# Kernel optimization log

Hardware: AMD Instinct MI355X
Metric: run time of the kernel (lower is better)

The kernel has to match this reference:

```python
import jax, jax.numpy as jnp
import numpy as np

# ---- module geometry ----
BULK = 64          # bulk (J2) integration points, 3 comps each
COH = 32           # cohesive integration points, 2 comps each
LS = BULK * 3 + COH * 2  # = 256, material layer width

# ---- J2 plasticity material constants (plane-stress, linear isotropic hardening) ----
E_MOD = 200.0
NU = 0.3
SY0 = 2.0
HARD = 10.0
G_MOD = E_MOD / (2.0 * (1.0 + NU))
_c = E_MOD / (1.0 - NU * NU)
C_EL = np.array([[_c, _c * NU, 0.0], [_c * NU, _c, 0.0], [0.0, 0.0, _c * (1.0 - NU) / 2.0]], dtype=np.float32)
C_INV = np.linalg.inv(C_EL).astype(np.float32)

# ---- Turon cohesive-zone constants (bilinear damage law) ----
K_PEN = 50.0       # penalty stiffness
DELTA0 = 0.1       # damage-onset effective jump
DELTAF = 1.0       # full-failure effective jump


def j2_update(eps, epsp, epbar):
    # eps, epsp: [B,P,3]; epbar: [B,P]. Radial-return with linear hardening.
    sig_tr = jnp.einsum('bpi,ji->bpj', eps - epsp, jnp.asarray(C_EL))
    s1, s2, s12 = sig_tr[..., 0], sig_tr[..., 1], sig_tr[..., 2]
    seq = jnp.sqrt(jnp.maximum(s1 * s1 - s1 * s2 + s2 * s2 + 3.0 * s12 * s12, 1e-12))
    f = seq - (SY0 + HARD * epbar)
    plastic = f > 0.0
    dep = jnp.where(plastic, f / (3.0 * G_MOD + HARD), 0.0)
    r = (SY0 + HARD * (epbar + dep)) / seq
    sig = jnp.where(plastic[..., None], r[..., None] * sig_tr, sig_tr)
    epsp_new = jnp.where(plastic[..., None], eps - jnp.einsum('bpj,ij->bpi', sig, jnp.asarray(C_INV)), epsp)
    return sig, epsp_new, epbar + dep


def coh_update(jump, hist):
    # jump: [B,P,2] (normal, shear); hist: [B,P] max effective jump (damage history).
    dn, ds = jump[..., 0], jump[..., 1]
    lam = jnp.sqrt(jnp.maximum(jnp.maximum(dn, 0.0) ** 2 + ds * ds, 1e-12))
    hist_new = jnp.maximum(hist, lam)
    dmg = jnp.clip(DELTAF * (hist_new - DELTA0) / (jnp.maximum(hist_new, 1e-12) * (DELTAF - DELTA0)), 0.0, 1.0)
    tn = K_PEN * dn * jnp.where(dn > 0.0, 1.0 - dmg, 1.0)  # compression is undamaged
    ts = (1.0 - dmg) * K_PEN * ds
    return jnp.stack([tn, ts], axis=-1), hist_new


def setup_inputs() -> dict:
    key = jax.random.key(0)
    k1, k2, k3 = jax.random.split(key, 3)
    x = jax.random.normal(k1, (256, 1024, 16), dtype=jnp.float32)
    W1 = jax.random.normal(k2, (LS, 16), dtype=jnp.float32) * 0.1
    W2 = jax.random.normal(k3, (16, LS), dtype=jnp.float32) * 0.1
    return {"x": x, "W1": W1, "W2": W2}


def reference(x, W1, W2):
    B, T, F = x.shape
    # fc1 applied to every (batch, time) slice (original loops; here one GEMM)
    h = jnp.einsum('btf,lf->btl', x, W1)  # [B,T,LS]
    h_t = jnp.transpose(h, (1, 0, 2))     # [T,B,LS] for the time scan

    epsp0 = jnp.zeros((B, BULK, 3), dtype=x.dtype)
    epbar0 = jnp.zeros((B, BULK), dtype=x.dtype)
    hist0 = jnp.zeros((B, COH), dtype=x.dtype)

    def step(carry, ht):
        epsp, epbar, hist = carry
        eps = ht[:, : BULK * 3].reshape(B, BULK, 3)
        jmp = ht[:, BULK * 3:].reshape(B, COH, 2)
        sig, epsp, epbar = j2_update(eps, epsp, epbar)   # update + commit per step
        trac, hist = coh_update(jmp, hist)
        y = jnp.concatenate([sig.reshape(B, -1), trac.reshape(B, -1)], axis=-1)
        return (epsp, epbar, hist), y

    _, ys = jax.lax.scan(step, (epsp0, epbar0, hist0), h_t)  # [T,B,LS]
    ys = jnp.transpose(ys, (1, 0, 2))  # [B,T,LS]
    # softLayer fc2: linear with softplus-constrained (non-negative) weights
    out = jnp.einsum('btl,ol->bto', ys, jax.nn.softplus(W2))
    return out
```

## Files before the change

### kernel.cpp

```cpp
#include <hip/hip_runtime.h>
#include <cmath>
#include <cstdint>

#define BATCH  256
#define TT     1024
#define FIN    16
#define TC     32
#define NCHUNK (TT / TC)
#define SROW   328
#define YSS    336

typedef __attribute__((ext_vector_type(8))) short short8;
typedef __attribute__((ext_vector_type(4))) float floatx4;

__device__ __forceinline__ unsigned short f2bf_rne(float f) {
    union { float f; unsigned int i; } v; v.f = f;
    unsigned int b = v.i;
    return (unsigned short)((b + 0x7FFFu + ((b >> 16) & 1u)) >> 16);
}
__device__ __forceinline__ float u2f(unsigned int u) {
    union { unsigned int i; float f; } v; v.i = u; return v.f;
}

#define BARRIER() asm volatile("s_waitcnt lgkmcnt(0)\n\ts_barrier" ::: "memory")

#define MC00   219.78021978021977f
#define MC01   65.93406593406593f
#define MC22   76.92307692307692f
#define MSY0   2.0f
#define AK     0.958466453674121406f
#define BK     0.041533546325878594f


__global__ __launch_bounds__(512, 1)
void fused_mat_kernel(const float* __restrict__ x,
                      const float* __restrict__ w1,
                      const float* __restrict__ w2,
                      float* __restrict__ out)
{
    __shared__ __attribute__((aligned(16))) float          s_h[2][TC][SROW];
    __shared__ __attribute__((aligned(16))) unsigned short s_y[2][TC][YSS];

    const int tid  = threadIdx.x;
    const int b    = blockIdx.x;
    const int lane = tid & 63;
    const int wv   = tid >> 6;
    const int m    = lane & 15;
    const int q    = lane >> 4;

    const size_t xrow = (size_t)b * TT;

    const bool isG     = (wv == 3) | (wv == 4) | (wv == 7);
    const int  hw      = (wv == 3) ? 0 : (wv == 4) ? 1 : 2;
    const int  nbase   = hw * 8;
    const int  nfrag   = (hw == 2) ? 4 : 8;
    const bool useDelta = (hw < 2);

    short8 wfrag[8];
    short8 vf[10];
    uint4  rxc[2][2], rxp[2][2];

    auto emit = [&](const short8* af, float* dst) {
        #pragma unroll
        for (int mt = 0; mt < 2; ++mt) {
            float* drow = dst + (mt * 16 + m) * SROW + q * 4 + nbase * 16;
            #pragma unroll
            for (int j = 0; j < 8; ++j) {
                if (j < nfrag) {
                    floatx4 acc = {0.f, 0.f, 0.f, 0.f};
                    acc = __builtin_amdgcn_mfma_f32_16x16x32_bf16(wfrag[j], af[mt], acc, 0, 0, 0);
                    *(floatx4*)(drow + j * 16) = acc;
                }
            }
        }
    };

    if (isG) {
        #pragma unroll
        for (int j = 0; j < 8; ++j) {
            short8 fr;
            #pragma unroll
            for (int jj = 0; jj < 8; ++jj) fr[jj] = 0;
            if (j < nfrag) {
                const int n = nbase + j;
                #pragma unroll
                for (int jj = 0; jj < 8; ++jj) {
                    float v = 0.f;
                    if (q < 2) {
                        const int f = q * 8 + jj;
                        if (n < 16) {
                            const int lp = n * 16 + m, c = lp >> 2, cm = lp & 3;
                            if (cm < 3) {
                                const float wa  = w1[(3 * c + 0) * FIN + f];
                                const float wb  = w1[(3 * c + 1) * FIN + f];
                                const float wcc = w1[(3 * c + 2) * FIN + f];
                                v = (cm == 0) ? fmaf(MC01, wb, MC00 * wa)
                                  : (cm == 1) ? fmaf(MC00, wb, MC01 * wa)
                                              : MC22 * wcc;
                            }
                        } else {
                            v = w1[(192 + (n - 16) * 16 + m) * FIN + f];
                        }
                    }
                    fr[jj] = (short)f2bf_rne(v);
                }
            }
            wfrag[j] = fr;
        }
        short8 af0[2];
        #pragma unroll
        for (int mt = 0; mt < 2; ++mt) {
            #pragma unroll
            for (int j = 0; j < 8; ++j) {
                float val = 0.f;
                if (q < 2) {
                    const int rowB = mt * 16 + m;
                    const float xc = x[(xrow + rowB) * FIN + q * 8 + j];
                    float xp = 0.f;
                    if (rowB > 0) xp = x[(xrow + rowB - 1) * FIN + q * 8 + j];
                    val = useDelta ? (xc - xp) : xc;
                }
                af0[mt][j] = (short)f2bf_rne(val);
            }
        }
        if (q < 2) {
            #pragma unroll
            for (int mt = 0; mt < 2; ++mt) {
                const int rowB = TC + mt * 16 + m;
                const float* xc = x + (xrow + rowB) * FIN + q * 8;
                const float* xp = x + (xrow + rowB - 1) * FIN + q * 8;
                rxc[mt][0] = *(const uint4*)xc;  rxc[mt][1] = *(const uint4*)(xc + 4);
                rxp[mt][0] = *(const uint4*)xp;  rxp[mt][1] = *(const uint4*)(xp + 4);
            }
        }
        emit(af0, &s_h[0][0][0]);
    } else if (wv == 5 || wv == 6) {
        #pragma unroll
        for (int ks = 0; ks < 10; ++ks) {
            #pragma unroll
            for (int j = 0; j < 8; ++j) {
                const int p = ks * 32 + q * 8 + j;
                unsigned short v = 0;
                if (p < 256) {
                    const int comp = p & 3;
                    if (comp < 3) {
                        const int l = 3 * (p >> 2) + comp;
                        float xv = w2[m * 256 + l];
                        float sp = fmaxf(xv, 0.0f) + log1pf(expf(-fabsf(xv)));
                        v = f2bf_rne(sp);
                    }
                } else {
                    const int l = p - 64;
                    float xv = w2[m * 256 + l];
                    float sp = fmaxf(xv, 0.0f) + log1pf(expf(-fabsf(xv)));
                    v = f2bf_rne(sp);
                }
                vf[ks][j] = (short)v;
            }
        }
    }

    float sg0 = 0.f, sg1 = 0.f, sg2 = 0.f, syv = MSY0, pre = AK * MSY0;
    float hist = 0.f;

    __syncthreads();

    for (int i = 0; i <= NCHUNK; ++i) {
        if (wv < 2) {
            if (i < NCHUNK && lane < 32) {
                const int p = wv * 32 + lane;
                const float* hb = &s_h[i & 1][0][0] + 4 * p;
                unsigned short* yb = &s_y[i & 1][0][0] + 4 * p;
                floatx4 dvv[TC];
                #pragma unroll
                for (int t = 0; t < TC; ++t) dvv[t] = *(const floatx4*)(hb + t * SROW);
                #pragma unroll
                for (int t = 0; t < TC; ++t) {
                    const floatx4 dv = dvv[t];
                    const float t0 = sg0 + dv.x, t1 = sg1 + dv.y, t2 = sg2 + dv.z;
                    const float s01 = t0 - t1;
                    const float u   = t2 * t2;
                    const float w3  = fmaf(u, 2.0f, u);
                    const float bb  = fmaf(t1, t1, w3);
                    const float qq  = fmaxf(fmaf(t0, s01, bb), 1e-12f);
                    const float rs  = __builtin_amdgcn_rsqf(qq);
                    const float seq = qq * rs;
                    const float rr  = fminf(fmaf(pre, rs, BK), 1.0f);
                    sg0 = rr * t0; sg1 = rr * t1; sg2 = rr * t2;
                    syv = fmaxf(syv, fmaf(BK, seq, pre));
                    pre = AK * syv;
                    unsigned int r0, r1;
                    asm("v_cvt_pk_bf16_f32 %0, %1, %2" : "=v"(r0) : "v"(sg0), "v"(sg1));
                    asm("v_cvt_pk_bf16_f32 %0, %1, %2" : "=v"(r1) : "v"(sg2), "v"(sg2));
                    uint2 pk; pk.x = r0; pk.y = r1;
                    *(uint2*)(yb + t * YSS) = pk;
                }
            }
        } else if (wv == 2) {
            if (i < NCHUNK && lane < 32) {
                const float* hc = &s_h[i & 1][0][0] + 256 + 2 * lane;
                unsigned short* yc = &s_y[i & 1][0][0] + 256 + 2 * lane;
                float2 jvv[TC];
                #pragma unroll
                for (int t = 0; t < TC; ++t) jvv[t] = *(const float2*)(hc + t * SROW);
                #pragma unroll
                for (int t = 0; t < TC; ++t) {
                    const float dn = jvv[t].x, ds = jvv[t].y;
                    const float dnp = fmaxf(dn, 0.0f);
                    const float lam = __builtin_amdgcn_sqrtf(fmaxf(fmaf(dnp, dnp, ds * ds), 1e-12f));
                    hist = fmaxf(hist, lam);
                    float dmg = (hist - 0.1f) * __builtin_amdgcn_rcpf(hist * 0.9f);
                    dmg = fminf(fmaxf(dmg, 0.0f), 1.0f);
                    const float om = 1.0f - dmg;
                    const float tn = 50.0f * dn * (dn > 0.0f ? om : 1.0f);
                    const float ts = om * 50.0f * ds;
                    unsigned int r;
                    asm("v_cvt_pk_bf16_f32 %0, %1, %2" : "=v"(r) : "v"(tn), "v"(ts));
                    *(unsigned int*)(yc + t * YSS) = r;
                }
            }
        } else if (isG) {
            if (i + 1 < NCHUNK) {
                short8 af[2];
                #pragma unroll
                for (int mt = 0; mt < 2; ++mt) {
                    const unsigned int wc[8] = {rxc[mt][0].x, rxc[mt][0].y, rxc[mt][0].z, rxc[mt][0].w,
                                                rxc[mt][1].x, rxc[mt][1].y, rxc[mt][1].z, rxc[mt][1].w};
                    const unsigned int wp[8] = {rxp[mt][0].x, rxp[mt][0].y, rxp[mt][0].z, rxp[mt][0].w,
                                                rxp[mt][1].x, rxp[mt][1].y, rxp[mt][1].z, rxp[mt][1].w};
                    #pragma unroll
                    for (int j = 0; j < 8; ++j) {
                        unsigned short v = 0;
                        if (q < 2) {
                            const float xc = u2f(wc[j]), xp = u2f(wp[j]);
                            const float val = useDelta ? (xc - xp) : xc;
                            v = f2bf_rne(val);
                        }
                        af[mt][j] = (short)v;
                    }
                }
                if (i + 2 < NCHUNK && q < 2) {
                    #pragma unroll
                    for (int mt = 0; mt < 2; ++mt) {
                        const int rowB = (i + 2) * TC + mt * 16 + m;
                        const float* xc = x + (xrow + rowB) * FIN + q * 8;
                        const float* xp = x + (xrow + rowB - 1) * FIN + q * 8;
                        rxc[mt][0] = *(const uint4*)xc;  rxc[mt][1] = *(const uint4*)(xc + 4);
                        rxp[mt][0] = *(const uint4*)xp;  rxp[mt][1] = *(const uint4*)(xp + 4);
                    }
                }
                emit(af, &s_h[(i + 1) & 1][0][0]);
            }
        } else {
            if (i >= 1) {
                const int mt = wv - 5;
                const int tb = (i - 1) * TC;
                const unsigned short* yb = &s_y[(i - 1) & 1][0][0];
                floatx4 a0 = {0.f, 0.f, 0.f, 0.f};
                floatx4 a1 = {0.f, 0.f, 0.f, 0.f};
                #pragma unroll
                for (int ks = 0; ks < 5; ++ks) {
                    const short8* yp = (const short8*)(yb + (mt * 16 + m) * YSS + ks * 32 + q * 8);
                    a0 = __builtin_amdgcn_mfma_f32_16x16x32_bf16(*yp, vf[ks], a0, 0, 0, 0);
                }
                #pragma unroll
                for (int ks = 5; ks < 10; ++ks) {
                    const short8* yp = (const short8*)(yb + (mt * 16 + m) * YSS + ks * 32 + q * 8);
                    a1 = __builtin_amdgcn_mfma_f32_16x16x32_bf16(*yp, vf[ks], a1, 0, 0, 0);
                }
                #pragma unroll
                for (int r = 0; r < 4; ++r)
                    out[(xrow + tb + mt * 16 + q * 4 + r) * FIN + m] = a0[r] + a1[r];
            }
        }
        BARRIER();
    }
}

extern "C" void kernel_launch(void* const* d_in, const int* in_sizes, int n_in,
                              void* d_out, int out_size, void* d_ws, size_t ws_size,
                              hipStream_t stream) {
    const float* x  = (const float*)d_in[0];
    const float* w1 = (const float*)d_in[1];
    const float* w2 = (const float*)d_in[2];
    float* out = (float*)d_out;
    fused_mat_kernel<<<BATCH, 512, 0, stream>>>(x, w1, w2, out);
}
```

Before: 145.3 us.

## Rebalance wave roles: one full J2 wave, four GEMM waves, streamed LDS loads

The J2 bulk update moves from two half-occupied waves (32 lanes each) into a single full 64-lane wave. The fc1 GEMM work is spread across four waves with five fragments each instead of three uneven waves, and each wave builds both delta and raw x operands. The J2 recurrence is reformulated to carry the trial stress and scale factor, which drops one clamp. Both recurrence waves now stream LDS reads through an 8-deep ring buffer instead of preloading all 32 timesteps, and they raise wave priority with s_setprio during the serial loop. The goal is to shorten the serial critical path and lower register pressure, at the cost of extra per-step issue inside one wave and more bf16 conversions on the GEMM waves.

```diff
diff --git a/kernel.cpp b/kernel.cpp
--- a/kernel.cpp
+++ b/kernel.cpp
@@ -50,77 +50,68 @@
 
     const size_t xrow = (size_t)b * TT;
 
-    const bool isG     = (wv == 3) | (wv == 4) | (wv == 7);
-    const int  hw      = (wv == 3) ? 0 : (wv == 4) ? 1 : 2;
-    const int  nbase   = hw * 8;
-    const int  nfrag   = (hw == 2) ? 4 : 8;
-    const bool useDelta = (hw < 2);
-
-    short8 wfrag[8];
+    const bool isG   = (wv == 2) | (wv == 3) | (wv == 6) | (wv == 7);
+    const int  hw    = (wv == 2) ? 0 : (wv == 3) ? 1 : (wv == 6) ? 2 : 3;
+    const int  nbase = hw * 5;
+
+    short8 wfrag[5];
     short8 vf[10];
     uint4  rxc[2][2], rxp[2][2];
 
-    auto emit = [&](const short8* af, float* dst) {
+    auto emit = [&](const short8* axv, const short8* adxv, float* dst) {
         #pragma unroll
         for (int mt = 0; mt < 2; ++mt) {
             float* drow = dst + (mt * 16 + m) * SROW + q * 4 + nbase * 16;
             #pragma unroll
+            for (int j = 0; j < 5; ++j) {
+                const int n = nbase + j;
+                floatx4 acc = {0.f, 0.f, 0.f, 0.f};
+                acc = __builtin_amdgcn_mfma_f32_16x16x32_bf16(
+                        wfrag[j], (n < 16) ? adxv[mt] : axv[mt], acc, 0, 0, 0);
+                *(floatx4*)(drow + j * 16) = acc;
+            }
+        }
+    };
+
+    if (isG) {
+        #pragma unroll
+        for (int j = 0; j < 5; ++j) {
+            const int n = nbase + j;
+            #pragma unroll
+            for (int jj = 0; jj < 8; ++jj) {
+                float v = 0.f;
+                if (q < 2) {
+                    const int f = q * 8 + jj;
+                    if (n < 16) {
+                        const int lp = n * 16 + m, c = lp >> 2, cm = lp & 3;
+                        if (cm < 3) {
+                            const float wa  = w1[(3 * c + 0) * FIN + f];
+                            const float wb  = w1[(3 * c + 1) * FIN + f];
+                            const float wcc = w1[(3 * c + 2) * FIN + f];
+                            v = (cm == 0) ? fmaf(MC01, wb, MC00 * wa)
+                              : (cm == 1) ? fmaf(MC00, wb, MC01 * wa)
+                                          : MC22 * wcc;
+                        }
+                    } else {
+                        v = w1[(192 + (n - 16) * 16 + m) * FIN + f];
+                    }
+                }
+                wfrag[j][jj] = (short)f2bf_rne(v);
+            }
+        }
+        short8 ax0[2], adx0[2];
+        #pragma unroll
+        for (int mt = 0; mt < 2; ++mt) {
+            #pragma unroll
             for (int j = 0; j < 8; ++j) {
-                if (j < nfrag) {
-                    floatx4 acc = {0.f, 0.f, 0.f, 0.f};
-                    acc = __builtin_amdgcn_mfma_f32_16x16x32_bf16(wfrag[j], af[mt], acc, 0, 0, 0);
-                    *(floatx4*)(drow + j * 16) = acc;
-                }
-            }
-        }
-    };
-
-    if (isG) {
-        #pragma unroll
-        for (int j = 0; j < 8; ++j) {
-            short8 fr;
-            #pragma unroll
-            for (int jj = 0; jj < 8; ++jj) fr[jj] = 0;
-            if (j < nfrag) {
-                const int n = nbase + j;
-                #pragma unroll
-                for (int jj = 0; jj < 8; ++jj) {
-                    float v = 0.f;
-                    if (q < 2) {
-                        const int f = q * 8 + jj;
-                        if (n < 16) {
-                            const int lp = n * 16 + m, c = lp >> 2, cm = lp & 3;
-                            if (cm < 3) {
-                                const float wa  = w1[(3 * c + 0) * FIN + f];
-                                const float wb  = w1[(3 * c + 1) * FIN + f];
-                                const float wcc = w1[(3 * c + 2) * FIN + f];
-                                v = (cm == 0) ? fmaf(MC01, wb, MC00 * wa)
-                                  : (cm == 1) ? fmaf(MC00, wb, MC01 * wa)
-                                              : MC22 * wcc;
-                            }
-                        } else {
-                            v = w1[(192 + (n - 16) * 16 + m) * FIN + f];
-                        }
-                    }
-                    fr[jj] = (short)f2bf_rne(v);
-                }
-            }
-            wfrag[j] = fr;
-        }
-        short8 af0[2];
-        #pragma unroll
-        for (int mt = 0; mt < 2; ++mt) {
-            #pragma unroll
-            for (int j = 0; j < 8; ++j) {
-                float val = 0.f;
+                float xc = 0.f, xp = 0.f;
                 if (q < 2) {
                     const int rowB = mt * 16 + m;
-                    const float xc = x[(xrow + rowB) * FIN + q * 8 + j];
-                    float xp = 0.f;
+                    xc = x[(xrow + rowB) * FIN + q * 8 + j];
                     if (rowB > 0) xp = x[(xrow + rowB - 1) * FIN + q * 8 + j];
-                    val = useDelta ? (xc - xp) : xc;
-                }
-                af0[mt][j] = (short)f2bf_rne(val);
+                }
+                ax0[mt][j]  = (short)f2bf_rne(xc);
+                adx0[mt][j] = (short)f2bf_rne(xc - xp);
             }
         }
         if (q < 2) {
@@ -133,8 +124,8 @@
                 rxp[mt][0] = *(const uint4*)xp;  rxp[mt][1] = *(const uint4*)(xp + 4);
             }
         }
-        emit(af0, &s_h[0][0][0]);
-    } else if (wv == 5 || wv == 6) {
+        emit(ax0, adx0, &s_h[0][0][0]);
+    } else if (wv == 4 || wv == 5) {
         #pragma unroll
         for (int ks = 0; ks < 10; ++ks) {
             #pragma unroll
@@ -160,52 +151,59 @@
         }
     }
 
-    float sg0 = 0.f, sg1 = 0.f, sg2 = 0.f, syv = MSY0, pre = AK * MSY0;
+    float tt0 = 0.f, tt1 = 0.f, tt2 = 0.f, rr = 1.0f, syv = MSY0, pre = AK * MSY0;
     float hist = 0.f;
 
     __syncthreads();
 
     for (int i = 0; i <= NCHUNK; ++i) {
-        if (wv < 2) {
-            if (i < NCHUNK && lane < 32) {
-                const int p = wv * 32 + lane;
-                const float* hb = &s_h[i & 1][0][0] + 4 * p;
-                unsigned short* yb = &s_y[i & 1][0][0] + 4 * p;
-                floatx4 dvv[TC];
-                #pragma unroll
-                for (int t = 0; t < TC; ++t) dvv[t] = *(const floatx4*)(hb + t * SROW);
+        if (wv == 0) {
+            if (i < NCHUNK) {
+                const float* hb = &s_h[i & 1][0][0] + 4 * lane;
+                unsigned short* yb = &s_y[i & 1][0][0] + 4 * lane;
+                floatx4 dbuf[8];
+                #pragma unroll
+                for (int p = 0; p < 8; ++p) dbuf[p] = *(const floatx4*)(hb + p * SROW);
+                __builtin_amdgcn_s_setprio(1);
                 #pragma unroll
                 for (int t = 0; t < TC; ++t) {
-                    const floatx4 dv = dvv[t];
-                    const float t0 = sg0 + dv.x, t1 = sg1 + dv.y, t2 = sg2 + dv.z;
-                    const float s01 = t0 - t1;
-                    const float u   = t2 * t2;
-                    const float w3  = fmaf(u, 2.0f, u);
-                    const float bb  = fmaf(t1, t1, w3);
-                    const float qq  = fmaxf(fmaf(t0, s01, bb), 1e-12f);
+                    const floatx4 dv = dbuf[t & 7];
+                    if (t + 8 < TC) dbuf[t & 7] = *(const floatx4*)(hb + (t + 8) * SROW);
+                    tt0 = fmaf(rr, tt0, dv.x);
+                    tt1 = fmaf(rr, tt1, dv.y);
+                    tt2 = fmaf(rr, tt2, dv.z);
+                    const float s01 = tt0 - tt1;
+                    const float u   = tt2 * tt2;
+                    const float w3  = fmaf(u, 3.0f, 1e-12f);
+                    const float bb  = fmaf(tt1, tt1, w3);
+                    const float qq  = fmaf(tt0, s01, bb);
                     const float rs  = __builtin_amdgcn_rsqf(qq);
                     const float seq = qq * rs;
-                    const float rr  = fminf(fmaf(pre, rs, BK), 1.0f);
-                    sg0 = rr * t0; sg1 = rr * t1; sg2 = rr * t2;
+                    rr  = fminf(fmaf(pre, rs, BK), 1.0f);
                     syv = fmaxf(syv, fmaf(BK, seq, pre));
                     pre = AK * syv;
+                    const float sg0 = rr * tt0, sg1 = rr * tt1, sg2 = rr * tt2;
                     unsigned int r0, r1;
                     asm("v_cvt_pk_bf16_f32 %0, %1, %2" : "=v"(r0) : "v"(sg0), "v"(sg1));
                     asm("v_cvt_pk_bf16_f32 %0, %1, %2" : "=v"(r1) : "v"(sg2), "v"(sg2));
                     uint2 pk; pk.x = r0; pk.y = r1;
                     *(uint2*)(yb + t * YSS) = pk;
                 }
-            }
-        } else if (wv == 2) {
+                __builtin_amdgcn_s_setprio(0);
+            }
+        } else if (wv == 1) {
             if (i < NCHUNK && lane < 32) {
                 const float* hc = &s_h[i & 1][0][0] + 256 + 2 * lane;
                 unsigned short* yc = &s_y[i & 1][0][0] + 256 + 2 * lane;
-                float2 jvv[TC];
-                #pragma unroll
-                for (int t = 0; t < TC; ++t) jvv[t] = *(const float2*)(hc + t * SROW);
+                float2 jbuf[8];
+                #pragma unroll
+                for (int p = 0; p < 8; ++p) jbuf[p] = *(const float2*)(hc + p * SROW);
+                __builtin_amdgcn_s_setprio(1);
                 #pragma unroll
                 for (int t = 0; t < TC; ++t) {
-                    const float dn = jvv[t].x, ds = jvv[t].y;
+                    const float2 jv = jbuf[t & 7];
+                    if (t + 8 < TC) jbuf[t & 7] = *(const float2*)(hc + (t + 8) * SROW);
+                    const float dn = jv.x, ds = jv.y;
                     const float dnp = fmaxf(dn, 0.0f);
                     const float lam = __builtin_amdgcn_sqrtf(fmaxf(fmaf(dnp, dnp, ds * ds), 1e-12f));
                     hist = fmaxf(hist, lam);
@@ -218,10 +216,11 @@
                     asm("v_cvt_pk_bf16_f32 %0, %1, %2" : "=v"(r) : "v"(tn), "v"(ts));
                     *(unsigned int*)(yc + t * YSS) = r;
                 }
+                __builtin_amdgcn_s_setprio(0);
             }
         } else if (isG) {
             if (i + 1 < NCHUNK) {
-                short8 af[2];
+                short8 ax[2], adx[2];
                 #pragma unroll
                 for (int mt = 0; mt < 2; ++mt) {
                     const unsigned int wc[8] = {rxc[mt][0].x, rxc[mt][0].y, rxc[mt][0].z, rxc[mt][0].w,
@@ -230,13 +229,14 @@
                                                 rxp[mt][1].x, rxp[mt][1].y, rxp[mt][1].z, rxp[mt][1].w};
                     #pragma unroll
                     for (int j = 0; j < 8; ++j) {
-                        unsigned short v = 0;
+                        unsigned short va = 0, vd = 0;
                         if (q < 2) {
                             const float xc = u2f(wc[j]), xp = u2f(wp[j]);
-                            const float val = useDelta ? (xc - xp) : xc;
-                            v = f2bf_rne(val);
+                            va = f2bf_rne(xc);
+                            vd = f2bf_rne(xc - xp);
                         }
-                        af[mt][j] = (short)v;
+                        ax[mt][j]  = (short)va;
+                        adx[mt][j] = (short)vd;
                     }
                 }
                 if (i + 2 < NCHUNK && q < 2) {
@@ -249,11 +249,11 @@
                         rxp[mt][0] = *(const uint4*)xp;  rxp[mt][1] = *(const uint4*)(xp + 4);
                     }
                 }
-                emit(af, &s_h[(i + 1) & 1][0][0]);
+                emit(ax, adx, &s_h[(i + 1) & 1][0][0]);
             }
         } else {
             if (i >= 1) {
-                const int mt = wv - 5;
+                const int mt = wv - 4;
                 const int tb = (i - 1) * TC;
                 const unsigned short* yb = &s_y[(i - 1) & 1][0][0];
                 floatx4 a0 = {0.f, 0.f, 0.f, 0.f};
```

Measured after the change: 185.1 us. 27.3% more time.
